# Kernel optimization log

Measured on AMD Instinct MI355X. Metric: run time of the kernel, lower is better.

The kernel has to match this reference:

```python
import jax, jax.numpy as jnp
import numpy as np

L = 4        # num_blocks
D = 512      # d_model
H = 8        # num_heads
DFF = 2048   # d_ff
EPS = 1.1920929e-07  # torch RMSNorm default eps = finfo(fp32).eps


def setup_inputs() -> dict:
    key = jax.random.key(0)
    ks = jax.random.split(key, 12)
    B, S = 4, 1024
    s = 0.02
    return {
        "x": jax.random.normal(ks[0], (B, S, D), jnp.float32),
        "col_ids": jax.random.randint(ks[1], (B, S), 0, 32),
        "row_ids": jax.random.randint(ks[2], (B, S), 0, 128),
        "nbr_ids": jax.random.randint(ks[3], (B, S), 0, 64),
        # per-block, per-relation attention weights (nn.Linear: y = x @ W.T)
        "Wq": jax.random.normal(ks[4], (L, 4, D, D), jnp.float32) * s,
        "Wk": jax.random.normal(ks[5], (L, 4, D, D), jnp.float32) * s,
        "Wv": jax.random.normal(ks[6], (L, 4, D, D), jnp.float32) * s,
        "Wo": jax.random.normal(ks[7], (L, 4, D, D), jnp.float32) * s,
        # SwiGLU FFN weights per block
        "W1": jax.random.normal(ks[8], (L, DFF, D), jnp.float32) * s,
        "W3": jax.random.normal(ks[9], (L, DFF, D), jnp.float32) * s,
        "W2": jax.random.normal(ks[10], (L, D, DFF), jnp.float32) * s,
        # RMSNorm scales: 4 attn norms + 1 ffn norm per block + final norm_out
        "g_attn": jnp.ones((L, 4, D), jnp.float32),
        "g_ffn": jnp.ones((L, D), jnp.float32),
        "g_out": jnp.ones((D,), jnp.float32),
    }


def _rms(x, g):
    return x * jax.lax.rsqrt(jnp.mean(x * x, axis=-1, keepdims=True) + EPS) * g


def _attn(x, wq, wk, wv, wo, mask):
    # x: [B,S,D]; mask: [B,S,S] bool (True = attend) or None for full attention
    B, S, _ = x.shape
    hd = D // H
    scale = 1.0 / np.sqrt(hd).astype(np.float32)
    q = (x @ wq.T).reshape(B, S, H, hd).transpose(0, 2, 1, 3)  # bhsd
    k = (x @ wk.T).reshape(B, S, H, hd).transpose(0, 2, 1, 3)
    v = (x @ wv.T).reshape(B, S, H, hd).transpose(0, 2, 1, 3)
    sc = jnp.einsum('bhqd,bhkd->bhqk', q, k) * scale
    if mask is not None:
        sc = jnp.where(mask[:, None, :, :], sc, jnp.float32(-1e30))
    a = jax.nn.softmax(sc, axis=-1)
    o = jnp.einsum('bhqk,bhkd->bhqd', a, v).transpose(0, 2, 1, 3).reshape(B, S, D)
    return o @ wo.T


def reference(x, col_ids, row_ids, nbr_ids, Wq, Wk, Wv, Wo, W1, W3, W2, g_attn, g_ffn, g_out):
    # relation order in RelationalBlock: col, feat, nbr, full
    masks = [ids[:, :, None] == ids[:, None, :] for ids in (col_ids, row_ids, nbr_ids)] + [None]
    for l in range(L):
        for r in range(4):
            x = x + _attn(_rms(x, g_attn[l, r]), Wq[l, r], Wk[l, r], Wv[l, r], Wo[l, r], masks[r])
        h = _rms(x, g_ffn[l])
        x = x + (jax.nn.silu(h @ W1[l].T) * (h @ W3[l].T)) @ W2[l].T
    return _rms(x, g_out)
```

## Files before the change

kernel.cpp:

```cpp
#include <hip/hip_runtime.h>
#include <hip/hip_bf16.h>


typedef __attribute__((ext_vector_type(4))) float f32x4;
typedef __attribute__((ext_vector_type(8))) short s16x8;
typedef __attribute__((ext_vector_type(4))) short s16x4;

#define SEQ 1024
#define DM 512
#define MTOT 4096
#define EPSV 1.1920929e-07f
#define LOG2E 1.44269504088896f

static __device__ __forceinline__ float b2f(short s) {
  unsigned u = ((unsigned)(unsigned short)s) << 16;
  return __builtin_bit_cast(float, u);
}
static __device__ __forceinline__ short f2b(float f) {
  unsigned u = __builtin_bit_cast(unsigned, f);
  u = (u + 0x7fffu + ((u >> 16) & 1u)) >> 16;
  return (short)(unsigned short)u;
}

#define MFMA_BF16(a, b, c) __builtin_amdgcn_mfma_f32_16x16x32_bf16((a), (b), (c), 0, 0, 0)
#define GLLDS(gp, lp)                                                                        \
  __builtin_amdgcn_global_load_lds((const __attribute__((address_space(1))) unsigned*)(gp),  \
                                   (__attribute__((address_space(3))) unsigned*)(lp), 16, 0, 0)
#define GLLDS4(gp, lp)                                                                       \
  __builtin_amdgcn_global_load_lds((const __attribute__((address_space(1))) unsigned*)(gp),  \
                                   (__attribute__((address_space(3))) unsigned*)(lp), 4, 0, 0)

__global__ void cvt_place(const f32x4* __restrict__ src, s16x4* __restrict__ dst, int n4,
                          int shift, int stride4, int off4, float scale) {
  int i = blockIdx.x * 256 + threadIdx.x;
  if (i >= n4) return;
  f32x4 v = src[i];
  s16x4 o;
  o[0] = f2b(v[0] * scale); o[1] = f2b(v[1] * scale);
  o[2] = f2b(v[2] * scale); o[3] = f2b(v[3] * scale);
  int c = i >> shift, r = i & ((1 << shift) - 1);
  dst[(size_t)c * stride4 + off4 + r] = o;
}

__global__ void cvt_w13(const f32x4* __restrict__ src, s16x4* __restrict__ dst, int n4, int off) {
  int i = blockIdx.x * 256 + threadIdx.x;
  if (i >= n4) return;
  f32x4 v = src[i];
  s16x4 o;
  o[0] = f2b(v[0]); o[1] = f2b(v[1]); o[2] = f2b(v[2]); o[3] = f2b(v[3]);
  int srcrow = i >> 7, r = i & 127;
  int l = srcrow >> 11, n = srcrow & 2047;
  int dstrow = l * 4096 + n * 2 + off;
  dst[(size_t)dstrow * 128 + r] = o;
}

template<bool F32OUT>
__global__ void rmsnorm_kernel(const float* __restrict__ x, const float* __restrict__ g,
                               void* __restrict__ outp) {
  int row = blockIdx.x * 4 + (threadIdx.x >> 6);
  int lane = threadIdx.x & 63;
  const float* xr = x + (size_t)row * DM + lane * 8;
  f32x4 a = *(const f32x4*)xr;
  f32x4 b = *(const f32x4*)(xr + 4);
  float ss = a[0]*a[0]+a[1]*a[1]+a[2]*a[2]+a[3]*a[3]+b[0]*b[0]+b[1]*b[1]+b[2]*b[2]+b[3]*b[3];
#pragma unroll
  for (int m = 1; m < 64; m <<= 1) ss += __shfl_xor(ss, m, 64);
  float sc = rsqrtf(ss * (1.0f / DM) + EPSV);
  const float* gp = g + lane * 8;
  if (F32OUT) {
    float* o = (float*)outp + (size_t)row * DM + lane * 8;
    f32x4 o0, o1;
#pragma unroll
    for (int j = 0; j < 4; j++) { o0[j] = a[j] * sc * gp[j]; o1[j] = b[j] * sc * gp[4 + j]; }
    *(f32x4*)o = o0;
    *(f32x4*)(o + 4) = o1;
  } else {
    s16x8 o;
#pragma unroll
    for (int j = 0; j < 4; j++) { o[j] = f2b(a[j] * sc * gp[j]); o[4 + j] = f2b(b[j] * sc * gp[4 + j]); }
    *(s16x8*)((short*)outp + (size_t)row * DM + lane * 8) = o;
  }
}

template<int AR, int AC, int FUSE>
__global__ __launch_bounds__(256) void gemm_bt(const short* __restrict__ A, const short* __restrict__ W,
                                               short* __restrict__ outb, float* __restrict__ outf,
                                               short* __restrict__ vtb, int N, int K) {
  constexpr int BM = AR * 32;
  constexpr int BN = AC * 32;
  __shared__ short As[BM * 32];
  __shared__ short Bs[BN * 32];
  const int tid = threadIdx.x;
  const int lane = tid & 63;
  const int w = tid >> 6;
  const int wr = w >> 1, wc = w & 1;
  const int m0 = blockIdx.x * BM, n0 = blockIdx.y * BN;
  f32x4 acc[AR][AC] = {};
  for (int k = 0; k < K; k += 32) {
    __syncthreads();
#pragma unroll
    for (int i = 0; i < BM / 64; i++) {
      int s = i * 256 + tid;
      int row = s >> 2, gl = s & 3, gd = gl ^ ((row >> 1) & 3);
      GLLDS(A + (size_t)(m0 + row) * K + k + gd * 8, (char*)As + (i * 256 + w * 64) * 16);
    }
#pragma unroll
    for (int i = 0; i < BN / 64; i++) {
      int s = i * 256 + tid;
      int row = s >> 2, gl = s & 3, gd = gl ^ ((row >> 1) & 3);
      GLLDS(W + (size_t)(n0 + row) * K + k + gd * 8, (char*)Bs + (i * 256 + w * 64) * 16);
    }
    __syncthreads();
    s16x8 af[AR], bf[AC];
#pragma unroll
    for (int i = 0; i < AR; i++) {
      int row = wr * AR * 16 + i * 16 + (lane & 15);
      int gl = (lane >> 4) ^ ((row >> 1) & 3);
      af[i] = *(const s16x8*)(As + row * 32 + gl * 8);
    }
#pragma unroll
    for (int j = 0; j < AC; j++) {
      int row = wc * AC * 16 + j * 16 + (lane & 15);
      int gl = (lane >> 4) ^ ((row >> 1) & 3);
      bf[j] = *(const s16x8*)(Bs + row * 32 + gl * 8);
    }
#pragma unroll
    for (int i = 0; i < AR; i++)
#pragma unroll
      for (int j = 0; j < AC; j++)
        acc[i][j] = MFMA_BF16(af[i], bf[j], acc[i][j]);
  }
#pragma unroll
  for (int i = 0; i < AR; i++) {
    int rbase = m0 + wr * AR * 16 + i * 16 + (lane >> 4) * 4;
#pragma unroll
    for (int j = 0; j < AC; j++) {
      int col = n0 + wc * AC * 16 + j * 16 + (lane & 15);
      if (FUSE == 2 && col >= 1024) {
        int bbv = rbase >> 10, s = rbase & 1023;
        int c = col - 1024, hhv = c >> 6, d = c & 63;
        int o = (s & 63) >> 2;
        int gg = o & 3, h2 = (o >> 2) & 1, q32 = o >> 3;
        int pnew = q32 * 8 + gg * 2 + h2;
        s16x4 o4;
#pragma unroll
        for (int r = 0; r < 4; r++) o4[r] = f2b(acc[i][j][r]);
        *(s16x4*)(vtb + (((size_t)(bbv * 8 + hhv) * 64 + d) << 10) + (s & ~63) + pnew * 4) = o4;
      } else if (FUSE == 3) {
#pragma unroll
        for (int r = 0; r < 4; r++) {
          float own = acc[i][j][r];
          float other = __shfl_xor(own, 1, 64);
          float sv = own / (1.0f + __expf(-own));
          if (!(lane & 1))
            outb[(size_t)(rbase + r) * (N >> 1) + (col >> 1)] = f2b(sv * other);
        }
      } else {
#pragma unroll
        for (int r = 0; r < 4; r++) {
          size_t idx = (size_t)(rbase + r) * N + col;
          if (FUSE == 1) outf[idx] += acc[i][j][r];
          else           outb[idx] = f2b(acc[i][j][r]);
        }
      }
    }
  }
}

__global__ __launch_bounds__(512) void attn_kernel(const short* __restrict__ qkv, const short* __restrict__ vt,
                                                   const int* __restrict__ ids, short* __restrict__ Ob) {
  const int bh = blockIdx.x;
  const int bb = bh >> 3, hh = bh & 7;
  const int q0 = blockIdx.y * 128;
  const int tid = threadIdx.x, lane = tid & 63, w = tid >> 6;
  const int g = lane >> 4, qi = lane & 15;
  __shared__ short Kl[128 * 64];
  __shared__ short Vl[64 * 128];
  __shared__ int Kid[128];
  const short* kbase = qkv + 512 + hh * 64;
  const short* vbase = vt + (size_t)bh * 64 * SEQ;
  s16x8 qf0, qf1;
  {
    int qrow = q0 + w * 16 + qi;
    const short* qp = qkv + (size_t)(bb * SEQ + qrow) * 1536 + hh * 64 + g * 8;
    qf0 = *(const s16x8*)qp;
    qf1 = *(const s16x8*)(qp + 32);
  }
  int qid = 0;
  if (ids) qid = ids[bb * SEQ + q0 + w * 16 + qi];
  float m_ = -1e30f, l_ = 0.f;
  f32x4 oacc[4] = {};

  for (int kt = 0; kt < SEQ; kt += 128) {
    __syncthreads();
#pragma unroll
    for (int i = 0; i < 2; i++) {
      int s = i * 512 + tid;
      int row = s >> 3, gl = s & 7, gd = gl ^ (row & 7);
      GLLDS(kbase + (size_t)(bb * SEQ + kt + row) * 1536 + gd * 8, (char*)Kl + (i * 512 + w * 64) * 16);
    }
#pragma unroll
    for (int i = 0; i < 2; i++) {
      int s = i * 512 + tid;
      int d = s >> 4, gl = s & 15, gd = gl ^ (d & 7);
      GLLDS(vbase + (size_t)d * SEQ + kt + gd * 8, (char*)Vl + (i * 512 + w * 64) * 16);
    }
    if (ids && w < 2) GLLDS4(ids + bb * SEQ + kt + w * 64 + lane, (char*)Kid + w * 256);
    __syncthreads();
    f32x4 sc[8];
#pragma unroll
    for (int kc = 0; kc < 8; kc++) {
      int krow = kc * 16 + qi;
      s16x8 kf0 = *(const s16x8*)(Kl + krow * 64 + ((g ^ (krow & 7)) * 8));
      s16x8 kf1 = *(const s16x8*)(Kl + krow * 64 + (((4 + g) ^ (krow & 7)) * 8));
      f32x4 s4 = {};
      s4 = MFMA_BF16(kf0, qf0, s4);
      s4 = MFMA_BF16(kf1, qf1, s4);
      sc[kc] = s4;
    }
    float p[8][4];
#pragma unroll
    for (int kc = 0; kc < 8; kc++)
#pragma unroll
      for (int r = 0; r < 4; r++) p[kc][r] = sc[kc][r];
    if (ids) {
#pragma unroll
      for (int kc = 0; kc < 8; kc++) {
        int4 kid4 = *(const int4*)(Kid + kc * 16 + g * 4);
        if (kid4.x != qid) p[kc][0] = -1e30f;
        if (kid4.y != qid) p[kc][1] = -1e30f;
        if (kid4.z != qid) p[kc][2] = -1e30f;
        if (kid4.w != qid) p[kc][3] = -1e30f;
      }
    }
    float mx = fmaxf(fmaxf(p[0][0], p[0][1]), fmaxf(p[0][2], p[0][3]));
#pragma unroll
    for (int kc = 1; kc < 8; kc++)
      mx = fmaxf(mx, fmaxf(fmaxf(p[kc][0], p[kc][1]), fmaxf(p[kc][2], p[kc][3])));
    mx = fmaxf(mx, __shfl_xor(mx, 16, 64));
    mx = fmaxf(mx, __shfl_xor(mx, 32, 64));
    if (__any(mx > m_ + 8.f)) {
      float nm = fmaxf(m_, mx);
      float c = exp2f(m_ - nm);
      m_ = nm;
      l_ *= c;
#pragma unroll
      for (int r = 0; r < 4; r++) {
        float cr = __shfl(c, g * 4 + r, 16);
        oacc[0][r] *= cr; oacc[1][r] *= cr; oacc[2][r] *= cr; oacc[3][r] *= cr;
      }
    }
    float sum = 0.f;
#pragma unroll
    for (int kc = 0; kc < 8; kc++)
#pragma unroll
      for (int r = 0; r < 4; r++) {
        p[kc][r] = exp2f(p[kc][r] - m_);
        sum += p[kc][r];
      }
    sum += __shfl_xor(sum, 16, 64);
    sum += __shfl_xor(sum, 32, 64);
    l_ += sum;
#pragma unroll
    for (int kk = 0; kk < 2; kk++) {
      s16x8 pa, pb;
#pragma unroll
      for (int r = 0; r < 4; r++) {
        pa[r] = f2b(p[kk * 4 + 0][r]); pa[4 + r] = f2b(p[kk * 4 + 1][r]);
        pb[r] = f2b(p[kk * 4 + 2][r]); pb[4 + r] = f2b(p[kk * 4 + 3][r]);
      }
#pragma unroll
      for (int dt = 0; dt < 4; dt++) {
        int dl = dt * 16 + qi;
        const short* vr = Vl + dl * 128;
        s16x8 vf0 = *(const s16x8*)(vr + (kk * 8 + (g ^ (dl & 7))) * 8);
        s16x8 vf1 = *(const s16x8*)(vr + (kk * 8 + ((4 + g) ^ (dl & 7))) * 8);
        oacc[dt] = MFMA_BF16(pa, vf0, oacc[dt]);
        oacc[dt] = MFMA_BF16(pb, vf1, oacc[dt]);
      }
    }
  }
  const size_t obase = (size_t)(bb * SEQ) * DM + hh * 64;
#pragma unroll
  for (int r = 0; r < 4; r++) {
    float lr = __shfl(l_, g * 4 + r, 16);
    float inv = 1.0f / lr;
    int q = q0 + w * 16 + g * 4 + r;
#pragma unroll
    for (int dt = 0; dt < 4; dt++)
      Ob[obase + (size_t)q * DM + dt * 16 + qi] = f2b(oacc[dt][r] * inv);
  }
}

extern "C" void kernel_launch(void* const* d_in, const int* in_sizes, int n_in,
                              void* d_out, int out_size, void* d_ws, size_t ws_size,
                              hipStream_t stream) {
  const float* x_in  = (const float*)d_in[0];
  const int* col_ids = (const int*)d_in[1];
  const int* row_ids = (const int*)d_in[2];
  const int* nbr_ids = (const int*)d_in[3];
  const float* g_attn = (const float*)d_in[11];
  const float* g_ffn  = (const float*)d_in[12];
  const float* g_out  = (const float*)d_in[13];

  char* ws = (char*)d_ws;
  float* x   = (float*)(ws);
  short* h   = (short*)(ws + (size_t)(8u  << 20));
  short* qkv = (short*)(ws + (size_t)(12u << 20));
  short* vt  = (short*)(ws + (size_t)(24u << 20));
  short* ob  = (short*)(ws + (size_t)(28u << 20));
  short* fa  = (short*)(ws + (size_t)(44u << 20));
  short* wqkv = (short*)(ws + (size_t)(60u  << 20));
  short* wob  = (short*)(ws + (size_t)(84u  << 20));
  short* w13  = (short*)(ws + (size_t)(92u  << 20));
  short* w2b  = (short*)(ws + (size_t)(108u << 20));

  const int N4 = 1048576;
  cvt_place<<<4096, 256, 0, stream>>>((const f32x4*)d_in[4], (s16x4*)wqkv, N4, 16, 196608, 0, 0.125f * LOG2E);
  cvt_place<<<4096, 256, 0, stream>>>((const f32x4*)d_in[5], (s16x4*)wqkv, N4, 16, 196608, 65536, 1.0f);
  cvt_place<<<4096, 256, 0, stream>>>((const f32x4*)d_in[6], (s16x4*)wqkv, N4, 16, 196608, 131072, 1.0f);
  cvt_place<<<4096, 256, 0, stream>>>((const f32x4*)d_in[7], (s16x4*)wob,  N4, 20, 0, 0, 1.0f);
  cvt_w13<<<4096, 256, 0, stream>>>((const f32x4*)d_in[8], (s16x4*)w13, N4, 0);
  cvt_w13<<<4096, 256, 0, stream>>>((const f32x4*)d_in[9], (s16x4*)w13, N4, 1);
  cvt_place<<<4096, 256, 0, stream>>>((const f32x4*)d_in[10], (s16x4*)w2b, N4, 20, 0, 0, 1.0f);

  hipMemcpyAsync(x, x_in, (size_t)MTOT * DM * 4, hipMemcpyDeviceToDevice, stream);

  const int* idsarr[4] = {col_ids, row_ids, nbr_ids, nullptr};

  for (int l = 0; l < 4; l++) {
    for (int r = 0; r < 4; r++) {
      rmsnorm_kernel<false><<<1024, 256, 0, stream>>>(x, g_attn + (size_t)(l * 4 + r) * DM, (void*)h);
      size_t woff = (size_t)(l * 4 + r) * 1536 * DM;
      gemm_bt<4, 2, 2><<<dim3(32, 24), 256, 0, stream>>>(h, wqkv + woff, qkv, nullptr, vt, 1536, DM);
      attn_kernel<<<dim3(32, 8), 512, 0, stream>>>(qkv, vt, idsarr[r], ob);
      gemm_bt<2, 2, 1><<<dim3(64, 8), 256, 0, stream>>>(ob, wob + (size_t)(l * 4 + r) * DM * DM,
                                                        nullptr, x, nullptr, DM, DM);
    }
    rmsnorm_kernel<false><<<1024, 256, 0, stream>>>(x, g_ffn + (size_t)l * DM, (void*)h);
    gemm_bt<4, 4, 3><<<dim3(32, 32), 256, 0, stream>>>(h, w13 + (size_t)l * 4096 * DM, fa, nullptr, nullptr, 4096, DM);
    gemm_bt<2, 2, 1><<<dim3(64, 8), 256, 0, stream>>>(fa, w2b + (size_t)l * DM * 2048, nullptr, x, nullptr, DM, 2048);
  }
  rmsnorm_kernel<true><<<1024, 256, 0, stream>>>(x, g_out, d_out);
}
```

Measured before the change: 1.237 ms.

## Double-buffer LDS tiles in GEMM and attention kernels to overlap loads

Both the bf16 GEMM and the flash-attention kernel now keep two LDS buffers for their tiles (A/W tiles in the GEMM; K, V and the mask ids in attention). The global-to-LDS loads for the next k-tile are issued before the MFMA work on the current tile, and a single barrier per iteration replaces the previous two. The aim is to hide global load latency behind matrix compute. The cost is twice the LDS per block, which may reduce occupancy, notably for the 512-thread attention kernel. Correctness relies on the barrier also waiting for the outstanding async loads.

```diff
diff --git a/kernel.cpp b/kernel.cpp
--- a/kernel.cpp
+++ b/kernel.cpp
@@ -88,48 +88,60 @@
                                                short* __restrict__ vtb, int N, int K) {
   constexpr int BM = AR * 32;
   constexpr int BN = AC * 32;
-  __shared__ short As[BM * 32];
-  __shared__ short Bs[BN * 32];
+  __shared__ short As[2][BM * 32];
+  __shared__ short Bs[2][BN * 32];
   const int tid = threadIdx.x;
   const int lane = tid & 63;
   const int w = tid >> 6;
   const int wr = w >> 1, wc = w & 1;
   const int m0 = blockIdx.x * BM, n0 = blockIdx.y * BN;
   f32x4 acc[AR][AC] = {};
-  for (int k = 0; k < K; k += 32) {
-    __syncthreads();
-#pragma unroll
-    for (int i = 0; i < BM / 64; i++) {
-      int s = i * 256 + tid;
-      int row = s >> 2, gl = s & 3, gd = gl ^ ((row >> 1) & 3);
-      GLLDS(A + (size_t)(m0 + row) * K + k + gd * 8, (char*)As + (i * 256 + w * 64) * 16);
-    }
-#pragma unroll
-    for (int i = 0; i < BN / 64; i++) {
-      int s = i * 256 + tid;
-      int row = s >> 2, gl = s & 3, gd = gl ^ ((row >> 1) & 3);
-      GLLDS(W + (size_t)(n0 + row) * K + k + gd * 8, (char*)Bs + (i * 256 + w * 64) * 16);
-    }
-    __syncthreads();
+
+#define STAGE_GEMM(buf, kk)                                                                      \
+  {                                                                                              \
+    _Pragma("unroll")                                                                            \
+    for (int i = 0; i < BM / 64; i++) {                                                          \
+      int s = i * 256 + tid;                                                                     \
+      int row = s >> 2, gl = s & 3, gd = gl ^ ((row >> 1) & 3);                                  \
+      GLLDS(A + (size_t)(m0 + row) * K + (kk) + gd * 8, (char*)As[buf] + (i * 256 + w * 64) * 16);\
+    }                                                                                            \
+    _Pragma("unroll")                                                                            \
+    for (int i = 0; i < BN / 64; i++) {                                                          \
+      int s = i * 256 + tid;                                                                     \
+      int row = s >> 2, gl = s & 3, gd = gl ^ ((row >> 1) & 3);                                  \
+      GLLDS(W + (size_t)(n0 + row) * K + (kk) + gd * 8, (char*)Bs[buf] + (i * 256 + w * 64) * 16);\
+    }                                                                                            \
+  }
+
+  STAGE_GEMM(0, 0);
+  __syncthreads();
+  int cur = 0;
+  const int nt = K >> 5;
+  for (int t = 0; t < nt; ++t) {
+    if (t + 1 < nt) STAGE_GEMM(cur ^ 1, (t + 1) * 32);
     s16x8 af[AR], bf[AC];
 #pragma unroll
     for (int i = 0; i < AR; i++) {
       int row = wr * AR * 16 + i * 16 + (lane & 15);
       int gl = (lane >> 4) ^ ((row >> 1) & 3);
-      af[i] = *(const s16x8*)(As + row * 32 + gl * 8);
+      af[i] = *(const s16x8*)(As[cur] + row * 32 + gl * 8);
     }
 #pragma unroll
     for (int j = 0; j < AC; j++) {
       int row = wc * AC * 16 + j * 16 + (lane & 15);
       int gl = (lane >> 4) ^ ((row >> 1) & 3);
-      bf[j] = *(const s16x8*)(Bs + row * 32 + gl * 8);
+      bf[j] = *(const s16x8*)(Bs[cur] + row * 32 + gl * 8);
     }
 #pragma unroll
     for (int i = 0; i < AR; i++)
 #pragma unroll
       for (int j = 0; j < AC; j++)
         acc[i][j] = MFMA_BF16(af[i], bf[j], acc[i][j]);
-  }
+    __syncthreads();
+    cur ^= 1;
+  }
+#undef STAGE_GEMM
+
 #pragma unroll
   for (int i = 0; i < AR; i++) {
     int rbase = m0 + wr * AR * 16 + i * 16 + (lane >> 4) * 4;
@@ -174,9 +186,9 @@
   const int q0 = blockIdx.y * 128;
   const int tid = threadIdx.x, lane = tid & 63, w = tid >> 6;
   const int g = lane >> 4, qi = lane & 15;
-  __shared__ short Kl[128 * 64];
-  __shared__ short Vl[64 * 128];
-  __shared__ int Kid[128];
+  __shared__ short Kl[2][128 * 64];
+  __shared__ short Vl[2][64 * 128];
+  __shared__ int Kid[2][128];
   const short* kbase = qkv + 512 + hh * 64;
   const short* vbase = vt + (size_t)bh * 64 * SEQ;
   s16x8 qf0, qf1;
@@ -191,28 +203,35 @@
   float m_ = -1e30f, l_ = 0.f;
   f32x4 oacc[4] = {};
 
+#define STAGE_ATTN(buf, ktt)                                                                     \
+  {                                                                                              \
+    _Pragma("unroll")                                                                            \
+    for (int i = 0; i < 2; i++) {                                                                \
+      int s = i * 512 + tid;                                                                     \
+      int row = s >> 3, gl = s & 7, gd = gl ^ (row & 7);                                         \
+      GLLDS(kbase + (size_t)(bb * SEQ + (ktt) + row) * 1536 + gd * 8,                            \
+            (char*)Kl[buf] + (i * 512 + w * 64) * 16);                                           \
+    }                                                                                            \
+    _Pragma("unroll")                                                                            \
+    for (int i = 0; i < 2; i++) {                                                                \
+      int s = i * 512 + tid;                                                                     \
+      int d = s >> 4, gl = s & 15, gd = gl ^ (d & 7);                                            \
+      GLLDS(vbase + (size_t)d * SEQ + (ktt) + gd * 8, (char*)Vl[buf] + (i * 512 + w * 64) * 16); \
+    }                                                                                            \
+    if (ids && w < 2) GLLDS4(ids + bb * SEQ + (ktt) + w * 64 + lane, (char*)Kid[buf] + w * 256); \
+  }
+
+  STAGE_ATTN(0, 0);
+  __syncthreads();
+  int cur = 0;
   for (int kt = 0; kt < SEQ; kt += 128) {
-    __syncthreads();
-#pragma unroll
-    for (int i = 0; i < 2; i++) {
-      int s = i * 512 + tid;
-      int row = s >> 3, gl = s & 7, gd = gl ^ (row & 7);
-      GLLDS(kbase + (size_t)(bb * SEQ + kt + row) * 1536 + gd * 8, (char*)Kl + (i * 512 + w * 64) * 16);
-    }
-#pragma unroll
-    for (int i = 0; i < 2; i++) {
-      int s = i * 512 + tid;
-      int d = s >> 4, gl = s & 15, gd = gl ^ (d & 7);
-      GLLDS(vbase + (size_t)d * SEQ + kt + gd * 8, (char*)Vl + (i * 512 + w * 64) * 16);
-    }
-    if (ids && w < 2) GLLDS4(ids + bb * SEQ + kt + w * 64 + lane, (char*)Kid + w * 256);
-    __syncthreads();
+    if (kt + 128 < SEQ) STAGE_ATTN(cur ^ 1, kt + 128);
     f32x4 sc[8];
 #pragma unroll
     for (int kc = 0; kc < 8; kc++) {
       int krow = kc * 16 + qi;
-      s16x8 kf0 = *(const s16x8*)(Kl + krow * 64 + ((g ^ (krow & 7)) * 8));
-      s16x8 kf1 = *(const s16x8*)(Kl + krow * 64 + (((4 + g) ^ (krow & 7)) * 8));
+      s16x8 kf0 = *(const s16x8*)(Kl[cur] + krow * 64 + ((g ^ (krow & 7)) * 8));
+      s16x8 kf1 = *(const s16x8*)(Kl[cur] + krow * 64 + (((4 + g) ^ (krow & 7)) * 8));
       f32x4 s4 = {};
       s4 = MFMA_BF16(kf0, qf0, s4);
       s4 = MFMA_BF16(kf1, qf1, s4);
@@ -226,7 +245,7 @@
     if (ids) {
 #pragma unroll
       for (int kc = 0; kc < 8; kc++) {
-        int4 kid4 = *(const int4*)(Kid + kc * 16 + g * 4);
+        int4 kid4 = *(const int4*)(Kid[cur] + kc * 16 + g * 4);
         if (kid4.x != qid) p[kc][0] = -1e30f;
         if (kid4.y != qid) p[kc][1] = -1e30f;
         if (kid4.z != qid) p[kc][2] = -1e30f;
@@ -272,14 +291,17 @@
 #pragma unroll
       for (int dt = 0; dt < 4; dt++) {
         int dl = dt * 16 + qi;
-        const short* vr = Vl + dl * 128;
+        const short* vr = Vl[cur] + dl * 128;
         s16x8 vf0 = *(const s16x8*)(vr + (kk * 8 + (g ^ (dl & 7))) * 8);
         s16x8 vf1 = *(const s16x8*)(vr + (kk * 8 + ((4 + g) ^ (dl & 7))) * 8);
         oacc[dt] = MFMA_BF16(pa, vf0, oacc[dt]);
         oacc[dt] = MFMA_BF16(pb, vf1, oacc[dt]);
       }
     }
-  }
+    __syncthreads();
+    cur ^= 1;
+  }
+#undef STAGE_ATTN
   const size_t obase = (size_t)(bb * SEQ) * DM + hh * 64;
 #pragma unroll
   for (int r = 0; r < 4; r++) {
```

Result: faster. 1.167 ms (-5.7%).
